# Optimization experiments

Measured on AMD Instinct MI355X. Metric: run time of the kernel, lower is better.

## Reference

```python
import jax, jax.numpy as jnp
import numpy as np
from jax import lax

WSIZE = 11
SIGMA = 1.5
PAD = WSIZE // 2  # 5
C1 = 0.01 ** 2
C2 = 0.03 ** 2


def _gauss1d():
    x = np.arange(WSIZE) - WSIZE // 2
    g = np.exp(-(x.astype(np.float64) ** 2) / (2.0 * SIGMA ** 2))
    g = g / g.sum()
    return jnp.asarray(g, dtype=jnp.float32)


def _blur3d(x, g):
    """Replicate-pad by 5 on D/H/W then apply the separable 11x11x11 Gaussian.
    x: [N, 1, D, H, W]. Mathematically identical to the dense conv3d in the
    original (the 3D window is an exact outer product of the 1D Gaussian)."""
    xp = jnp.pad(x, ((0, 0), (0, 0), (PAD, PAD), (PAD, PAD), (PAD, PAD)), mode='edge')
    dn = ('NCDHW', 'OIDHW', 'NCDHW')
    for kshape in ((1, 1, WSIZE, 1, 1), (1, 1, 1, WSIZE, 1), (1, 1, 1, 1, WSIZE)):
        xp = lax.conv_general_dilated(xp, g.reshape(kshape), (1, 1, 1), 'VALID',
                                      dimension_numbers=dn)
    return xp


def _rerange(img):
    img = jnp.where(img.max() > 128.0, img / 255.0, img)
    img = jnp.where(img.min() < -0.5, (img + 1.0) / 2.0, img)
    return img


def setup_inputs() -> dict:
    key = jax.random.key(0)
    k1, k2 = jax.random.split(key)
    N, C, H, W = 4, 16, 512, 512
    pred = jax.random.uniform(k1, (N, C, H, W), dtype=jnp.float32)
    gt = jax.random.uniform(k2, (N, C, H, W), dtype=jnp.float32)
    return {"pred": pred, "gt": gt}


def reference(pred, gt):
    N = pred.shape[0]
    pred = _rerange(pred)
    gt = _rerange(gt)

    # ---- PSNR (range = 1.0, reduce='sum') ----
    mse = jnp.mean((pred - gt) ** 2, axis=(1, 2, 3))           # [N]
    psnr = jnp.sum(10.0 * jnp.log10(1.0 / mse))                # scalar

    # ---- 3D SSIM over [N,1,C,H,W] volumes ----
    g = _gauss1d()
    img = pred[:, None]                                        # [N,1,D,H,W]
    gtt = gt[:, None]
    mu1 = _blur3d(img, g)
    mu2 = _blur3d(gtt, g)
    mu1_sq = mu1 * mu1
    mu2_sq = mu2 * mu2
    mu1_mu2 = mu1 * mu2
    sigma1_sq = _blur3d(img * img, g) - mu1_sq
    sigma2_sq = _blur3d(gtt * gtt, g) - mu2_sq
    sigma12 = _blur3d(img * gtt, g) - mu1_mu2

    v1 = 2.0 * sigma12 + C2
    v2 = sigma1_sq + sigma2_sq + C2
    ssim_map = ((2.0 * mu1_mu2 + C1) * v1) / ((mu1_sq + mu2_sq + C1) * v2)
    ssim = jnp.sum(jnp.mean(ssim_map, axis=(1, 2, 3, 4)))      # reduce='sum'

    return psnr, ssim, N
```

## Files before the change

kernel.cpp:

```cpp
#include <hip/hip_runtime.h>
#include <cmath>


#define NB 4
#define DD 16
#define HH 512
#define WW 512
#define SLICE (HH * WW)
#define VOL (DD * SLICE)
#define C1F 0.0001f
#define C2F 0.0009f

#define TH 16
#define TW 16
#define SCOLS 26
#define NRP 13
#define PW 14
#define PLSTR 28
#define SDW (NRP * PLSTR)
#define TMW (TH * PW)
#define NTHR 256
#define SIT (NRP * SCOLS)
#define XTRA (SIT - NTHR)
#define HITEMS 104

typedef _Float16 h2v __attribute__((ext_vector_type(2)));

struct KArg {
  unsigned ge[6], go[6];
  float wlT[DD * DD];
};

__device__ inline float dot2h(unsigned a, unsigned b, float c) {
#if __has_builtin(__builtin_amdgcn_fdot2)
  return __builtin_amdgcn_fdot2(__builtin_bit_cast(h2v, a),
                                __builtin_bit_cast(h2v, b), c, false);
#else
  h2v av = __builtin_bit_cast(h2v, a), bv = __builtin_bit_cast(h2v, b);
  return fmaf((float)av.y, (float)bv.y, fmaf((float)av.x, (float)bv.x, c));
#endif
}
__device__ inline unsigned pkh(float a, float b) {
  return __builtin_bit_cast(unsigned, __builtin_amdgcn_cvt_pkrtz(a, b));
}
__device__ inline unsigned pk2sq(unsigned a) {
  h2v v = __builtin_bit_cast(h2v, a);
  v = v * v;
  return __builtin_bit_cast(unsigned, v);
}
__device__ inline int iclamp(int v, int lo, int hi) {
  return v < lo ? lo : (v > hi ? hi : v);
}

__device__ inline float block_sum256(float v) {
#pragma unroll
  for (int o = 32; o > 0; o >>= 1) v += __shfl_down(v, o, 64);
  __shared__ float r[4];
  if ((threadIdx.x & 63) == 0) r[threadIdx.x >> 6] = v;
  __syncthreads();
  float out = 0.f;
  if (threadIdx.x == 0) {
#pragma unroll
    for (int i = 0; i < 4; ++i) out += r[i];
  }
  __syncthreads();
  return out;
}

__global__ void zero_acc_k(float* acc) {
  if (threadIdx.x < 8) acc[threadIdx.x] = 0.f;
}

__global__ __launch_bounds__(NTHR, 3) void fused_k(
    const float* __restrict__ pred, const float* __restrict__ gt,
    float* __restrict__ acc, KArg ka) {
  __shared__ uint2 sd[SDW];
  __shared__ uint4 tmp[TMW];

  int b0 = blockIdx.x;
  int b = (b0 & 7) * ((NB * 1024) >> 3) + (b0 >> 3);
  int tile = b & 1023;
  int n = b >> 10;
  int th0 = (tile >> 5) * TH;
  int tw0 = (tile & 31) * TW;
  int t = threadIdx.x;

  int rp0 = t / SCOLS, x0 = t - rp0 * SCOLS;
  int gx0 = iclamp(tw0 + x0 - 5, 0, WW - 1);
  int go0a = iclamp(th0 + 2 * rp0 - 5, 0, HH - 1) * WW + gx0;
  int go0b = iclamp(th0 + 2 * rp0 - 4, 0, HH - 1) * WW + gx0;
  int w0i = (2 * rp0 + (x0 & 1)) * PW + (x0 >> 1);
  bool ox0 = (x0 >= 5) && (x0 < 5 + TW);
  float o0a = (ox0 && rp0 >= 3 && rp0 <= 10) ? 1.f : 0.f;
  float o0b = (ox0 && rp0 >= 2 && rp0 <= 9) ? 1.f : 0.f;
  int i1 = t + XTRA;
  bool has2 = (i1 >= NTHR);
  int rp1 = i1 / SCOLS, x1 = i1 - rp1 * SCOLS;
  int gx1 = iclamp(tw0 + x1 - 5, 0, WW - 1);
  int go1a = iclamp(th0 + 2 * rp1 - 5, 0, HH - 1) * WW + gx1;
  int go1b = iclamp(th0 + 2 * rp1 - 4, 0, HH - 1) * WW + gx1;
  int w1i = (2 * rp1 + (x1 & 1)) * PW + (x1 >> 1);
  bool ox1 = (x1 >= 5) && (x1 < 5 + TW);
  float o1a = (ox1 && rp1 >= 3 && rp1 <= 10) ? 1.f : 0.f;
  float o1b = (ox1 && rp1 >= 2 && rp1 <= 9) ? 1.f : 0.f;

  bool hasH = (t < HITEMS);
  int hm = t & 7, hcp = t >> 3;
  int hrd = hm * PLSTR + hcp;
  int hwr = (2 * hm) * PW + hcp;

  int wx = t & 15;
  int wrd = (t >> 4) * PW + (wx >> 1);
  unsigned cw[6];
#pragma unroll
  for (int J = 0; J < 6; ++J) cw[J] = (wx & 1) ? ka.go[J] : ka.ge[J];

  const float* pb = pred + (size_t)n * VOL;
  const float* qb = gt + (size_t)n * VOL;

  float p0a = pb[go0a], p0b = pb[go0b], q0a = qb[go0a], q0b = qb[go0b];
  float p1a = 0.f, p1b = 0.f, q1a = 0.f, q1b = 0.f;
  if (has2) { p1a = pb[go1a]; p1b = pb[go1b]; q1a = qb[go1a]; q1b = qb[go1b]; }

  float psnr = 0.f;
  float a0[DD], a1[DD], a2[DD], a3[DD];
#pragma unroll
  for (int j = 0; j < DD; ++j) { a0[j] = a1[j] = a2[j] = a3[j] = 0.f; }

#pragma unroll 1
  for (int d = 0; d < DD; ++d) {
    {
      float SA = p0a + q0a, DA = p0a - q0a;
      float SB = p0b + q0b, DB = p0b - q0b;
      psnr = fmaf(o0a, DA * DA, psnr);
      psnr = fmaf(o0b, DB * DB, psnr);
      sd[w0i] = make_uint2(pkh(SA, SB), pkh(DA, DB));
    }
    if (has2) {
      float SA = p1a + q1a, DA = p1a - q1a;
      float SB = p1b + q1b, DB = p1b - q1b;
      psnr = fmaf(o1a, DA * DA, psnr);
      psnr = fmaf(o1b, DB * DB, psnr);
      sd[w1i] = make_uint2(pkh(SA, SB), pkh(DA, DB));
    }
    __syncthreads();

    if (d < DD - 1) {
      const float* P = pb + (size_t)(d + 1) * SLICE;
      const float* Q = qb + (size_t)(d + 1) * SLICE;
      p0a = P[go0a]; p0b = P[go0b]; q0a = Q[go0a]; q0b = Q[go0b];
      if (has2) { p1a = P[go1a]; p1b = P[go1b]; q1a = Q[go1a]; q1b = Q[go1b]; }
    }

    if (hasH) {
      float e0[4] = {0, 0, 0, 0}, e1[4] = {0, 0, 0, 0};
      float r0[4] = {0, 0, 0, 0}, r1[4] = {0, 0, 0, 0};
#pragma unroll
      for (int J = 0; J < 6; ++J) {
        uint2 ve = sd[hrd + J * PLSTR];
        uint2 vo = sd[hrd + J * PLSTR + PW];
        unsigned ves = pk2sq(ve.x), ved = pk2sq(ve.y);
        unsigned vos = pk2sq(vo.x), vod = pk2sq(vo.y);
        unsigned cge = ka.ge[J], cgo = ka.go[J];
        e0[0] = dot2h(cge, ve.x, e0[0]); e0[1] = dot2h(cge, ve.y, e0[1]);
        e0[2] = dot2h(cge, ves, e0[2]);  e0[3] = dot2h(cge, ved, e0[3]);
        r0[0] = dot2h(cgo, ve.x, r0[0]); r0[1] = dot2h(cgo, ve.y, r0[1]);
        r0[2] = dot2h(cgo, ves, r0[2]);  r0[3] = dot2h(cgo, ved, r0[3]);
        e1[0] = dot2h(cge, vo.x, e1[0]); e1[1] = dot2h(cge, vo.y, e1[1]);
        e1[2] = dot2h(cge, vos, e1[2]);  e1[3] = dot2h(cge, vod, e1[3]);
        r1[0] = dot2h(cgo, vo.x, r1[0]); r1[1] = dot2h(cgo, vo.y, r1[1]);
        r1[2] = dot2h(cgo, vos, r1[2]);  r1[3] = dot2h(cgo, vod, r1[3]);
      }
      tmp[hwr] = make_uint4(pkh(e0[0], e1[0]), pkh(e0[1], e1[1]),
                            pkh(e0[2], e1[2]), pkh(e0[3], e1[3]));
      tmp[hwr + PW] = make_uint4(pkh(r0[0], r1[0]), pkh(r0[1], r1[1]),
                                 pkh(r0[2], r1[2]), pkh(r0[3], r1[3]));
    }
    __syncthreads();

    float w0 = 0.f, w1 = 0.f, w2 = 0.f, w3 = 0.f;
#pragma unroll
    for (int J = 0; J < 6; ++J) {
      uint4 v = tmp[wrd + J];
      w0 = dot2h(cw[J], v.x, w0); w1 = dot2h(cw[J], v.y, w1);
      w2 = dot2h(cw[J], v.z, w2); w3 = dot2h(cw[J], v.w, w3);
    }
    const float* wl = ka.wlT + d * DD;
#pragma unroll
    for (int o = 0; o < DD; ++o) {
      float w = wl[o];
      a0[o] = fmaf(w, w0, a0[o]);
      a1[o] = fmaf(w, w1, a1[o]);
      a2[o] = fmaf(w, w2, a2[o]);
      a3[o] = fmaf(w, w3, a3[o]);
    }
  }

  float ssum = 0.f;
#pragma unroll
  for (int j = 0; j < DD; ++j) {
    float Sb = a0[j], Db = a1[j], B1 = a2[j], B2 = a3[j];
    float SS = Sb * Sb, DDm = Db * Db;
    float m12_2 = (SS - DDm) * 0.5f;
    float msq   = (SS + DDm) * 0.5f;
    float Epq   = (B1 - B2) * 0.25f;
    float Esum  = (B1 + B2) * 0.5f;
    float sig12_2 = 2.f * Epq - m12_2;
    float svar    = Esum - msq;
    float num = (m12_2 + C1F) * (sig12_2 + C2F);
    float den = (msq + C1F) * (svar + C2F);
    ssum += num / den;
  }
  float bs = block_sum256(ssum);
  if (t == 0) atomicAdd(&acc[4 + n], bs);
  float bp = block_sum256(psnr);
  if (t == 0) atomicAdd(&acc[n], bp);
}

__global__ void final_k(const float* __restrict__ acc, float* __restrict__ out) {
  if (threadIdx.x == 0 && blockIdx.x == 0) {
    double psnr = 0.0, ssim = 0.0;
    for (int n = 0; n < NB; ++n) {
      double mse = (double)acc[n] / (double)VOL;
      psnr += 10.0 * log10(1.0 / mse);
      ssim += (double)acc[4 + n] / (double)VOL;
    }
    out[0] = (float)psnr;
    out[1] = (float)ssim;
    out[2] = (float)NB;
  }
}

static unsigned short f2h(float f) {
  union { float f; unsigned u; } v; v.f = f;
  unsigned u = v.u;
  unsigned s = (u >> 16) & 0x8000u;
  int e = (int)((u >> 23) & 0xff) - 127 + 15;
  unsigned m = u & 0x7fffffu;
  if (e <= 0) return (unsigned short)s;
  if (e >= 31) return (unsigned short)(s | 0x7c00u);
  unsigned h = ((unsigned)e << 10) | (m >> 13);
  unsigned rem = m & 0x1fffu;
  if (rem > 0x1000u || (rem == 0x1000u && (h & 1u))) h++;
  return (unsigned short)(s | h);
}
static float h2f(unsigned short h) {
  unsigned se = (h >> 10) & 0x1f, m = h & 0x3ffu, s = ((unsigned)h & 0x8000u) << 16;
  union { unsigned u; float f; } v;
  if (se == 0) { v.u = s; return v.f; }
  v.u = s | ((se - 15 + 127) << 23) | (m << 13);
  return v.f;
}

extern "C" void kernel_launch(void* const* d_in, const int* in_sizes, int n_in,
                              void* d_out, int out_size, void* d_ws, size_t ws_size,
                              hipStream_t stream) {
  const float* pred = (const float*)d_in[0];
  const float* gt = (const float*)d_in[1];
  float* acc = (float*)d_ws;

  double tt[11], s = 0.0;
  for (int i = 0; i < 11; ++i) {
    double x = i - 5;
    tt[i] = exp(-(x * x) / 4.5);
    s += tt[i];
  }
  float g[11];
  for (int i = 0; i < 11; ++i) g[i] = (float)(tt[i] / s);

  unsigned short hg[11];
  for (int i = 0; i < 11; ++i) hg[i] = f2h(g[i]);
  for (int pass = 0; pass < 3; ++pass) {
    double sum = 0.0;
    for (int i = 0; i < 11; ++i) sum += (double)h2f(hg[i]);
    hg[5] = f2h((float)((double)h2f(hg[5]) + (1.0 - sum)));
  }

  KArg ka;
  for (int j = 0; j < 5; ++j)
    ka.ge[j] = (unsigned)hg[2 * j] | ((unsigned)hg[2 * j + 1] << 16);
  ka.ge[5] = (unsigned)hg[10];
  ka.go[0] = ((unsigned)hg[0]) << 16;
  for (int j = 1; j < 6; ++j)
    ka.go[j] = (unsigned)hg[2 * j - 1] | ((unsigned)hg[2 * j] << 16);

  for (int o = 0; o < DD; ++o)
    for (int d = 0; d < DD; ++d) {
      float w = 0.f;
      for (int k = 0; k < 11; ++k) {
        int j = o + k - 5;
        j = j < 0 ? 0 : (j > 15 ? 15 : j);
        if (j == d) w += g[k];
      }
      ka.wlT[d * DD + o] = w;
    }

  zero_acc_k<<<1, 64, 0, stream>>>(acc);
  fused_k<<<NB * 1024, NTHR, 0, stream>>>(pred, gt, acc, ka);
  final_k<<<1, 1, 0, stream>>>(acc, (float*)d_out);
}
```

Baseline: 251.3 us.

## Double-buffer shared tiles to pipeline H and W passes with one barrier per slice

Double-buffers the staged input slice and the intermediate H-blurred tile in shared memory. Each iteration now writes the next slice, runs the W-pass for the previous slice and the H-pass for the current one, with a single barrier per depth step instead of two. The aim is to cut synchronisation stalls and let independent work overlap. It doubles LDS use and adds a prologue and epilogue, with possible register pressure under the launch bound.

```diff
diff --git a/kernel.cpp b/kernel.cpp
--- a/kernel.cpp
+++ b/kernel.cpp
@@ -74,8 +74,8 @@
 __global__ __launch_bounds__(NTHR, 3) void fused_k(
     const float* __restrict__ pred, const float* __restrict__ gt,
     float* __restrict__ acc, KArg ka) {
-  __shared__ uint2 sd[SDW];
-  __shared__ uint4 tmp[TMW];
+  __shared__ uint2 sd[2 * SDW];
+  __shared__ uint4 tmp[2 * TMW];
 
   int b0 = blockIdx.x;
   int b = (b0 & 7) * ((NB * 1024) >> 3) + (b0 >> 3);
@@ -118,38 +118,85 @@
   const float* pb = pred + (size_t)n * VOL;
   const float* qb = gt + (size_t)n * VOL;
 
+  float psnr = 0.f;
+  float a0[DD], a1[DD], a2[DD], a3[DD];
+#pragma unroll
+  for (int j = 0; j < DD; ++j) { a0[j] = a1[j] = a2[j] = a3[j] = 0.f; }
+
   float p0a = pb[go0a], p0b = pb[go0b], q0a = qb[go0a], q0b = qb[go0b];
   float p1a = 0.f, p1b = 0.f, q1a = 0.f, q1b = 0.f;
   if (has2) { p1a = pb[go1a]; p1b = pb[go1b]; q1a = qb[go1a]; q1b = qb[go1b]; }
-
-  float psnr = 0.f;
-  float a0[DD], a1[DD], a2[DD], a3[DD];
-#pragma unroll
-  for (int j = 0; j < DD; ++j) { a0[j] = a1[j] = a2[j] = a3[j] = 0.f; }
+  {
+    float SA = p0a + q0a, DA = p0a - q0a;
+    float SB = p0b + q0b, DB = p0b - q0b;
+    psnr = fmaf(o0a, DA * DA, psnr);
+    psnr = fmaf(o0b, DB * DB, psnr);
+    sd[w0i] = make_uint2(pkh(SA, SB), pkh(DA, DB));
+  }
+  if (has2) {
+    float SA = p1a + q1a, DA = p1a - q1a;
+    float SB = p1b + q1b, DB = p1b - q1b;
+    psnr = fmaf(o1a, DA * DA, psnr);
+    psnr = fmaf(o1b, DB * DB, psnr);
+    sd[w1i] = make_uint2(pkh(SA, SB), pkh(DA, DB));
+  }
+  {
+    const float* P = pb + SLICE;
+    const float* Q = qb + SLICE;
+    p0a = P[go0a]; p0b = P[go0b]; q0a = Q[go0a]; q0b = Q[go0b];
+    if (has2) { p1a = P[go1a]; p1b = P[go1b]; q1a = Q[go1a]; q1b = Q[go1b]; }
+  }
+  __syncthreads();
+
+  float ww0, ww1, ww2, ww3;
 
 #pragma unroll 1
   for (int d = 0; d < DD; ++d) {
-    {
-      float SA = p0a + q0a, DA = p0a - q0a;
-      float SB = p0b + q0b, DB = p0b - q0b;
-      psnr = fmaf(o0a, DA * DA, psnr);
-      psnr = fmaf(o0b, DB * DB, psnr);
-      sd[w0i] = make_uint2(pkh(SA, SB), pkh(DA, DB));
-    }
-    if (has2) {
-      float SA = p1a + q1a, DA = p1a - q1a;
-      float SB = p1b + q1b, DB = p1b - q1b;
-      psnr = fmaf(o1a, DA * DA, psnr);
-      psnr = fmaf(o1b, DB * DB, psnr);
-      sd[w1i] = make_uint2(pkh(SA, SB), pkh(DA, DB));
-    }
-    __syncthreads();
+    uint2* sdn = sd + ((d + 1) & 1) * SDW;
+    const uint2* sdc = sd + (d & 1) * SDW;
+    uint4* tmc = tmp + (d & 1) * TMW;
+    const uint4* tmr = tmp + ((d + 1) & 1) * TMW;
 
     if (d < DD - 1) {
-      const float* P = pb + (size_t)(d + 1) * SLICE;
-      const float* Q = qb + (size_t)(d + 1) * SLICE;
-      p0a = P[go0a]; p0b = P[go0b]; q0a = Q[go0a]; q0b = Q[go0b];
-      if (has2) { p1a = P[go1a]; p1b = P[go1b]; q1a = Q[go1a]; q1b = Q[go1b]; }
+      {
+        float SA = p0a + q0a, DA = p0a - q0a;
+        float SB = p0b + q0b, DB = p0b - q0b;
+        psnr = fmaf(o0a, DA * DA, psnr);
+        psnr = fmaf(o0b, DB * DB, psnr);
+        sdn[w0i] = make_uint2(pkh(SA, SB), pkh(DA, DB));
+      }
+      if (has2) {
+        float SA = p1a + q1a, DA = p1a - q1a;
+        float SB = p1b + q1b, DB = p1b - q1b;
+        psnr = fmaf(o1a, DA * DA, psnr);
+        psnr = fmaf(o1b, DB * DB, psnr);
+        sdn[w1i] = make_uint2(pkh(SA, SB), pkh(DA, DB));
+      }
+      if (d < DD - 2) {
+        const float* P = pb + (size_t)(d + 2) * SLICE;
+        const float* Q = qb + (size_t)(d + 2) * SLICE;
+        p0a = P[go0a]; p0b = P[go0b]; q0a = Q[go0a]; q0b = Q[go0b];
+        if (has2) { p1a = P[go1a]; p1b = P[go1b]; q1a = Q[go1a]; q1b = Q[go1b]; }
+      }
+    }
+
+    if (d >= 1) {
+      ww0 = 0.f; ww1 = 0.f; ww2 = 0.f; ww3 = 0.f;
+#pragma unroll
+      for (int J = 0; J < 6; ++J) {
+        uint4 v = tmr[wrd + J];
+        ww0 = dot2h(cw[J], v.x, ww0); ww1 = dot2h(cw[J], v.y, ww1);
+        ww2 = dot2h(cw[J], v.z, ww2); ww3 = dot2h(cw[J], v.w, ww3);
+      }
+      const float* wl = ka.wlT + (d - 1) * DD;
+#pragma unroll
+      for (int o = 0; o < DD; ++o) {
+        float w = wl[o];
+        a0[o] = fmaf(w, ww0, a0[o]);
+        a1[o] = fmaf(w, ww1, a1[o]);
+        a2[o] = fmaf(w, ww2, a2[o]);
+        a3[o] = fmaf(w, ww3, a3[o]);
+      }
     }
 
     if (hasH) {
@@ -157,8 +204,8 @@
       float r0[4] = {0, 0, 0, 0}, r1[4] = {0, 0, 0, 0};
 #pragma unroll
       for (int J = 0; J < 6; ++J) {
-        uint2 ve = sd[hrd + J * PLSTR];
-        uint2 vo = sd[hrd + J * PLSTR + PW];
+        uint2 ve = sdc[hrd + J * PLSTR];
+        uint2 vo = sdc[hrd + J * PLSTR + PW];
         unsigned ves = pk2sq(ve.x), ved = pk2sq(ve.y);
         unsigned vos = pk2sq(vo.x), vod = pk2sq(vo.y);
         unsigned cge = ka.ge[J], cgo = ka.go[J];
@@ -171,28 +218,32 @@
         r1[0] = dot2h(cgo, vo.x, r1[0]); r1[1] = dot2h(cgo, vo.y, r1[1]);
         r1[2] = dot2h(cgo, vos, r1[2]);  r1[3] = dot2h(cgo, vod, r1[3]);
       }
-      tmp[hwr] = make_uint4(pkh(e0[0], e1[0]), pkh(e0[1], e1[1]),
+      tmc[hwr] = make_uint4(pkh(e0[0], e1[0]), pkh(e0[1], e1[1]),
                             pkh(e0[2], e1[2]), pkh(e0[3], e1[3]));
-      tmp[hwr + PW] = make_uint4(pkh(r0[0], r1[0]), pkh(r0[1], r1[1]),
+      tmc[hwr + PW] = make_uint4(pkh(r0[0], r1[0]), pkh(r0[1], r1[1]),
                                  pkh(r0[2], r1[2]), pkh(r0[3], r1[3]));
     }
+
     __syncthreads();
-
-    float w0 = 0.f, w1 = 0.f, w2 = 0.f, w3 = 0.f;
+  }
+
+  {
+    const uint4* tmr = tmp + (15 & 1) * TMW;
+    ww0 = 0.f; ww1 = 0.f; ww2 = 0.f; ww3 = 0.f;
 #pragma unroll
     for (int J = 0; J < 6; ++J) {
-      uint4 v = tmp[wrd + J];
-      w0 = dot2h(cw[J], v.x, w0); w1 = dot2h(cw[J], v.y, w1);
-      w2 = dot2h(cw[J], v.z, w2); w3 = dot2h(cw[J], v.w, w3);
-    }
-    const float* wl = ka.wlT + d * DD;
+      uint4 v = tmr[wrd + J];
+      ww0 = dot2h(cw[J], v.x, ww0); ww1 = dot2h(cw[J], v.y, ww1);
+      ww2 = dot2h(cw[J], v.z, ww2); ww3 = dot2h(cw[J], v.w, ww3);
+    }
+    const float* wl = ka.wlT + 15 * DD;
 #pragma unroll
     for (int o = 0; o < DD; ++o) {
       float w = wl[o];
-      a0[o] = fmaf(w, w0, a0[o]);
-      a1[o] = fmaf(w, w1, a1[o]);
-      a2[o] = fmaf(w, w2, a2[o]);
-      a3[o] = fmaf(w, w3, a3[o]);
+      a0[o] = fmaf(w, ww0, a0[o]);
+      a1[o] = fmaf(w, ww1, a1[o]);
+      a2[o] = fmaf(w, ww2, a2[o]);
+      a3[o] = fmaf(w, ww3, a3[o]);
     }
   }
 
```

Result: no change. 254.8 us (+1.4%).
